# Kernel tuning notes

Measured on AMD Instinct MI355X. Metric: run time of the kernel, lower is better.

## Reference

```python
import jax, jax.numpy as jnp
import numpy as np

B, S, H = 32, 1024, 1024
W, K = 128, 6
NUM_HEADS = 16


def setup_inputs() -> dict:
    key = jax.random.key(0)
    k1, k2 = jax.random.split(key, 2)
    token_embeddings = jax.random.normal(k1, (B, S, H), dtype=jnp.float32)
    # nn.MultiheadAttention packed in_proj (q,k,v). v / out_proj never affect the
    # module output (attn_output is discarded), but we keep full-size params.
    in_proj_weight = jax.random.normal(k2, (3 * H, H), dtype=jnp.float32) * (1.0 / np.sqrt(H))
    in_proj_bias = jnp.zeros((3 * H,), dtype=jnp.float32)
    # Build ragged word->subtoken map as padded [B, W, K] indices + validity mask.
    # Words occupy disjoint contiguous slots (stride S//W = 8 >= K), matching the
    # disjointness the tokenizer guarantees in get_subtok_map.
    rng = np.random.default_rng(0)
    lengths = rng.integers(2, K + 1, size=(B, W))  # each kept word has >=2 subtokens
    stride = S // W
    base = (np.arange(W) * stride)[None, :, None] + np.arange(K)[None, None, :]
    base = np.broadcast_to(base, (B, W, K))
    mask = np.arange(K)[None, None, :] < lengths[:, :, None]
    idx = np.where(mask, base, 0)
    return {
        "token_embeddings": token_embeddings,
        "in_proj_weight": in_proj_weight,
        "in_proj_bias": in_proj_bias,
        "subtok_idx": jnp.asarray(idx, dtype=jnp.int32),
        "subtok_mask": jnp.asarray(mask),
        "num_heads": NUM_HEADS,
    }


def _merge(token_embeddings, in_proj_weight, in_proj_bias, subtok_idx, subtok_mask, num_heads):
    Bv, Sv, Hv = token_embeddings.shape
    Wv, Kv = subtok_idx.shape[1], subtok_idx.shape[2]
    hd = Hv // num_heads
    dtype = token_embeddings.dtype
    maskf = subtok_mask.astype(dtype)
    b_idx = jnp.arange(Bv)[:, None, None]
    sub = token_embeddings[b_idx, subtok_idx]                      # [B,W,K,H] gather
    x = (sub * maskf[..., None]).reshape(Bv * Wv, Kv, Hv)          # zero-padded groups
    # q,k projections (v / out_proj do not influence returned embeddings)
    qk = x @ in_proj_weight[: 2 * Hv].T + in_proj_bias[: 2 * Hv]
    q, k = qk[..., :Hv], qk[..., Hv:]
    q = q.reshape(-1, Kv, num_heads, hd).transpose(0, 2, 1, 3)     # [L,nh,K,hd]
    k = k.reshape(-1, Kv, num_heads, hd).transpose(0, 2, 1, 3)
    scores = jnp.einsum('lnqd,lnkd->lnqk', q, k) / jnp.asarray(np.sqrt(hd), dtype)
    m = maskf.reshape(-1, Kv)
    pair = m[:, :, None] * m[:, None, :]                           # [L,K,K] 0/1 float mask
    # torch adds float attn_mask to scores (it does NOT -inf mask here) -- faithful
    scores = scores + pair[:, None]
    attn = jax.nn.softmax(scores, axis=-1)
    w_mean = attn.mean(axis=1)                                     # avg over heads (need_weights)
    contrib = (pair * w_mean).sum(axis=1)                          # sum over query dim
    contrib = contrib / (contrib.sum(axis=-1, keepdims=True) + 1e-8)
    contrib = contrib.reshape(Bv, Wv, Kv)                          # zero at invalid k
    unified = jnp.einsum('bwkh,bwk->bwh', sub, contrib)
    # zero ALL subtoken positions of each word, then write merged vector at the
    # first subtoken index (equivalent to the torch in-place per-word loop since
    # word index sets are disjoint). Column Sv is a discard slot for padding.
    safe_idx = jnp.where(subtok_mask, subtok_idx, Sv)
    keep = jnp.ones((Bv, Sv + 1), dtype=dtype)
    keep = keep.at[b_idx, safe_idx].set(0.0)
    out = token_embeddings * keep[:, :Sv, None]
    out = jnp.concatenate([out, jnp.zeros((Bv, 1, Hv), dtype)], axis=1)
    first_idx = jnp.where(subtok_mask[:, :, 0], subtok_idx[:, :, 0], Sv)
    out = out.at[jnp.arange(Bv)[:, None], first_idx].set(unified)
    return out[:, :Sv]


def reference(token_embeddings, in_proj_weight, in_proj_bias, subtok_idx, subtok_mask, num_heads):
    return _merge(token_embeddings, in_proj_weight, in_proj_bias, subtok_idx, subtok_mask, num_heads)
```

## Files before the change

kernel.cpp:

```cpp
#include <hip/hip_runtime.h>
#include <hip/hip_bf16.h>
#include <stdint.h>
#include <stddef.h>

#define Bdim  32
#define Sdim  1024
#define Hdim  1024
#define Wdim  128
#define Ktok  6
#define NHEAD 16
#define HDdim 64
#define Lgrp  (Bdim*Wdim)
#define Mrows (Lgrp*Ktok)
#define Ncols (2*Hdim)
#define CVTROWS (Mrows + Ncols)

typedef __attribute__((ext_vector_type(8))) short short8;
typedef __attribute__((ext_vector_type(4))) short short4_t;
typedef __attribute__((ext_vector_type(4))) float floatx4;
typedef __hip_bfloat16 bf16_t;

typedef unsigned int u32_g __attribute__((address_space(1)));
typedef unsigned int u32_l __attribute__((address_space(3)));

__device__ __forceinline__ void gld_lds16(const void* g, void* l) {
    __builtin_amdgcn_global_load_lds((const u32_g*)g, (u32_l*)l, 16, 0, 0);
}

__device__ __forceinline__ float b2f(short s) {
    union { float f; unsigned u; } x; x.u = ((unsigned)(unsigned short)s) << 16; return x.f;
}

__device__ __forceinline__ short8 cvt8(const float4 lo, const float4 hi) {
    union { short8 s; bf16_t h[8]; } u;
    u.h[0] = __float2bfloat16(lo.x); u.h[1] = __float2bfloat16(lo.y);
    u.h[2] = __float2bfloat16(lo.z); u.h[3] = __float2bfloat16(lo.w);
    u.h[4] = __float2bfloat16(hi.x); u.h[5] = __float2bfloat16(hi.y);
    u.h[6] = __float2bfloat16(hi.z); u.h[7] = __float2bfloat16(hi.w);
    return u.s;
}

__global__ void gather_cvt(const float* __restrict__ TE, const float* __restrict__ Wt,
                           const int* __restrict__ sidx,
                           bf16_t* __restrict__ Xa, bf16_t* __restrict__ Wb)
{
    const int r = blockIdx.x;
    const int t = threadIdx.x;
    const float* src;
    bf16_t* dst;
    if (r < Mrows) {
        src = TE + ((size_t)(r/768)*Sdim + sidx[r])*Hdim;
        dst = Xa + (size_t)r*Hdim;
    } else {
        src = Wt + (size_t)(r - Mrows)*Hdim;
        dst = Wb + (size_t)(r - Mrows)*Hdim;
    }
    const float4 v = *(const float4*)(src + t*4);
    union { short4_t s; bf16_t h[4]; } u;
    u.h[0] = __float2bfloat16(v.x); u.h[1] = __float2bfloat16(v.y);
    u.h[2] = __float2bfloat16(v.z); u.h[3] = __float2bfloat16(v.w);
    *(short4_t*)(dst + t*4) = u.s;
}

__global__ __launch_bounds__(256, 2) void gemm_bf16(
    const bf16_t* __restrict__ Xa, const bf16_t* __restrict__ Wb,
    const float* __restrict__ bias, bf16_t* __restrict__ Cq)
{
    __shared__ __align__(16) bf16_t As[128*32];
    __shared__ __align__(16) bf16_t Bs[128*32];
    const int tid  = threadIdx.x;
    const int wv   = tid >> 6;
    const int lane = tid & 63;
    const int tileM = blockIdx.x * 128;
    const int tileN = blockIdx.y * 128;

    const int r0 = wv*32 + (lane>>2);
    const int r1 = r0 + 16;
    const int c8 = (lane&3)*8;

    const bf16_t* pA0 = Xa + (size_t)(tileM + r0)*Hdim + c8;
    const bf16_t* pA1 = Xa + (size_t)(tileM + r1)*Hdim + c8;
    const bf16_t* pB0 = Wb + (size_t)(tileN + r0)*Hdim + c8;
    const bf16_t* pB1 = Wb + (size_t)(tileN + r1)*Hdim + c8;
    bf16_t* lA0 = &As[r0*32 + c8];
    bf16_t* lA1 = &As[r1*32 + c8];
    bf16_t* lB0 = &Bs[r0*32 + c8];
    bf16_t* lB1 = &Bs[r1*32 + c8];

    const int wm = (wv & 1)*64;
    const int wn = (wv >> 1)*64;
    const int fr = lane & 15;
    const int fq = lane >> 4;

    floatx4 acc[4][4] = {};

    for (int k0 = 0; k0 < Hdim; k0 += 32) {
        gld_lds16(pA0 + k0, lA0);
        gld_lds16(pA1 + k0, lA1);
        gld_lds16(pB0 + k0, lB0);
        gld_lds16(pB1 + k0, lB1);
        __syncthreads();
        short8 a[4], b[4];
        #pragma unroll
        for (int mi = 0; mi < 4; mi++)
            a[mi] = *(const short8*)(const void*)&As[(wm + mi*16 + fr)*32 + fq*8];
        #pragma unroll
        for (int ni = 0; ni < 4; ni++)
            b[ni] = *(const short8*)(const void*)&Bs[(wn + ni*16 + fr)*32 + fq*8];
        #pragma unroll
        for (int mi = 0; mi < 4; mi++)
            #pragma unroll
            for (int ni = 0; ni < 4; ni++)
                acc[mi][ni] = __builtin_amdgcn_mfma_f32_16x16x32_bf16(
                    a[mi], b[ni], acc[mi][ni], 0, 0, 0);
        __syncthreads();
    }

    #pragma unroll
    for (int ni = 0; ni < 4; ni++) {
        const int col = tileN + wn + ni*16 + fr;
        const float bv = bias[col];
        #pragma unroll
        for (int mi = 0; mi < 4; mi++) {
            #pragma unroll
            for (int r = 0; r < 4; r++) {
                const int row = tileM + wm + mi*16 + fq*4 + r;
                Cq[(size_t)row * Ncols + col] = __float2bfloat16(acc[mi][ni][r] + bv);
            }
        }
    }
}

__global__ __launch_bounds__(256, 2) void gemm_qk(
    const float* __restrict__ TE, const float* __restrict__ Wt,
    const float* __restrict__ bias, const int* __restrict__ sidx,
    bf16_t* __restrict__ Cq)
{
    __shared__ __align__(16) bf16_t As[128*32];
    __shared__ __align__(16) bf16_t Bs[128*32];
    const int tid  = threadIdx.x;
    const int wv   = tid >> 6;
    const int lane = tid & 63;
    const int tileM = blockIdx.x * 128;
    const int tileN = blockIdx.y * 128;

    const int r0 = wv*32 + (lane>>2);
    const int r1 = r0 + 16;
    const int c8 = (lane&3)*8;

    const int m0 = tileM + r0;
    const int m1 = tileM + r1;
    const float* pA0 = TE + ((size_t)(m0/768)*Sdim + sidx[m0])*Hdim + c8;
    const float* pA1 = TE + ((size_t)(m1/768)*Sdim + sidx[m1])*Hdim + c8;
    const float* pB0 = Wt + (size_t)(tileN + r0)*Hdim + c8;
    const float* pB1 = Wt + (size_t)(tileN + r1)*Hdim + c8;
    bf16_t* lA0 = &As[r0*32 + c8];
    bf16_t* lA1 = &As[r1*32 + c8];
    bf16_t* lB0 = &Bs[r0*32 + c8];
    bf16_t* lB1 = &Bs[r1*32 + c8];

    const int wm = (wv & 1)*64;
    const int wn = (wv >> 1)*64;
    const int fr = lane & 15;
    const int fq = lane >> 4;

    floatx4 acc[4][4] = {};

    for (int k0 = 0; k0 < Hdim; k0 += 32) {
        const float4 a0l = *(const float4*)(pA0 + k0);
        const float4 a0h = *(const float4*)(pA0 + k0 + 4);
        const float4 a1l = *(const float4*)(pA1 + k0);
        const float4 a1h = *(const float4*)(pA1 + k0 + 4);
        const float4 b0l = *(const float4*)(pB0 + k0);
        const float4 b0h = *(const float4*)(pB0 + k0 + 4);
        const float4 b1l = *(const float4*)(pB1 + k0);
        const float4 b1h = *(const float4*)(pB1 + k0 + 4);
        *(short8*)(void*)lA0 = cvt8(a0l, a0h);
        *(short8*)(void*)lA1 = cvt8(a1l, a1h);
        *(short8*)(void*)lB0 = cvt8(b0l, b0h);
        *(short8*)(void*)lB1 = cvt8(b1l, b1h);
        __syncthreads();
        short8 a[4], b[4];
        #pragma unroll
        for (int mi = 0; mi < 4; mi++)
            a[mi] = *(const short8*)(const void*)&As[(wm + mi*16 + fr)*32 + fq*8];
        #pragma unroll
        for (int ni = 0; ni < 4; ni++)
            b[ni] = *(const short8*)(const void*)&Bs[(wn + ni*16 + fr)*32 + fq*8];
        #pragma unroll
        for (int mi = 0; mi < 4; mi++)
            #pragma unroll
            for (int ni = 0; ni < 4; ni++)
                acc[mi][ni] = __builtin_amdgcn_mfma_f32_16x16x32_bf16(
                    a[mi], b[ni], acc[mi][ni], 0, 0, 0);
        __syncthreads();
    }

    #pragma unroll
    for (int ni = 0; ni < 4; ni++) {
        const int col = tileN + wn + ni*16 + fr;
        const float bv = bias[col];
        #pragma unroll
        for (int mi = 0; mi < 4; mi++) {
            #pragma unroll
            for (int r = 0; r < 4; r++) {
                const int row = tileM + wm + mi*16 + fq*4 + r;
                Cq[(size_t)row * Ncols + col] = __float2bfloat16(acc[mi][ni][r] + bv);
            }
        }
    }
}

__global__ void copy_te(const uint4* __restrict__ src, uint4* __restrict__ dst, int n)
{
    int i = blockIdx.x * blockDim.x + threadIdx.x;
    const int stride = gridDim.x * blockDim.x;
    for (; i < n; i += stride) dst[i] = src[i];
}

__global__ __launch_bounds__(256) void attn_merge(
    const float* __restrict__ TE, const bf16_t* __restrict__ Cq,
    const float* __restrict__ bias, const int* __restrict__ sidx,
    float* __restrict__ out)
{
    __shared__ __align__(16) bf16_t qk[Ktok][Ncols];
    __shared__ float sc[NHEAD][Ktok][Ktok];
    __shared__ float cN[Ktok];
    __shared__ int   validS[Ktok];

    const int g   = blockIdx.x;
    const int b   = g >> 7;
    const int w   = g & (Wdim - 1);
    const int tid = threadIdx.x;

    if (tid < Ktok) {
        const int id = sidx[g*Ktok + tid];
        validS[tid] = (id != 0) || (w == 0 && tid == 0);
    }
    __syncthreads();

    int valid[Ktok], idxv[Ktok];
    #pragma unroll
    for (int kk = 0; kk < Ktok; kk++) { valid[kk] = validS[kk]; idxv[kk] = sidx[g*Ktok + kk]; }

    #pragma unroll
    for (int it = 0; it < Ktok; it++) {
        if (valid[it]) {
            *(short8*)(void*)&qk[it][tid*8] =
                *(const short8*)(const void*)&Cq[(size_t)(g*Ktok + it)*Ncols + tid*8];
        } else {
            const float4 lo = *(const float4*)(bias + tid*8);
            const float4 hi = *(const float4*)(bias + tid*8 + 4);
            *(short8*)(void*)&qk[it][tid*8] = cvt8(lo, hi);
        }
    }
    __syncthreads();

    for (int t = tid; t < NHEAD*Ktok*Ktok; t += 256) {
        const int n = t / (Ktok*Ktok);
        const int pr = t % (Ktok*Ktok);
        const int i = pr / Ktok, j = pr % Ktok;
        const bf16_t* qp = &qk[i][n*HDdim];
        const bf16_t* kp = &qk[j][Hdim + n*HDdim];
        float dot = 0.f;
        #pragma unroll
        for (int c = 0; c < 8; c++) {
            const short8 q8 = *(const short8*)(const void*)(qp + c*8);
            const short8 k8 = *(const short8*)(const void*)(kp + c*8);
            #pragma unroll
            for (int e = 0; e < 8; e++) dot += b2f(q8[e]) * b2f(k8[e]);
        }
        sc[n][i][j] = dot * 0.125f + ((valid[i] && valid[j]) ? 1.0f : 0.0f);
    }
    __syncthreads();

    if (tid < NHEAD*Ktok) {
        const int n = tid / Ktok, i = tid % Ktok;
        float mx = -1e30f;
        #pragma unroll
        for (int j = 0; j < Ktok; j++) mx = fmaxf(mx, sc[n][i][j]);
        float e[Ktok], sum = 0.f;
        #pragma unroll
        for (int j = 0; j < Ktok; j++) { e[j] = __expf(sc[n][i][j] - mx); sum += e[j]; }
        const float inv = 1.0f / sum;
        #pragma unroll
        for (int j = 0; j < Ktok; j++) sc[n][i][j] = e[j] * inv;
    }
    __syncthreads();

    if (tid == 0) {
        float cb[Ktok], tot = 0.f;
        #pragma unroll
        for (int j = 0; j < Ktok; j++) cb[j] = 0.f;
        #pragma unroll
        for (int i = 0; i < Ktok; i++) {
            if (!valid[i]) continue;
            #pragma unroll
            for (int j = 0; j < Ktok; j++) {
                if (!valid[j]) continue;
                float s = 0.f;
                #pragma unroll
                for (int n = 0; n < NHEAD; n++) s += sc[n][i][j];
                cb[j] += s * (1.0f/NHEAD);
            }
        }
        #pragma unroll
        for (int j = 0; j < Ktok; j++) tot += cb[j];
        const float inv = 1.0f / (tot + 1e-8f);
        #pragma unroll
        for (int j = 0; j < Ktok; j++) cN[j] = cb[j] * inv;
    }
    __syncthreads();

    float cw[Ktok];
    #pragma unroll
    for (int kk = 0; kk < Ktok; kk++) cw[kk] = cN[kk];

    const int c4 = tid * 4;
    const size_t rowOut = ((size_t)b*Sdim + idxv[0]) * Hdim;
    float4 u = {0.f, 0.f, 0.f, 0.f};
    #pragma unroll
    for (int kk = 0; kk < Ktok; kk++) {
        const float4 v = *(const float4*)(TE + ((size_t)b*Sdim + idxv[kk])*Hdim + c4);
        u.x += cw[kk]*v.x; u.y += cw[kk]*v.y; u.z += cw[kk]*v.z; u.w += cw[kk]*v.w;
    }
    *(float4*)(out + rowOut + c4) = u;

    const float4 z = {0.f, 0.f, 0.f, 0.f};
    #pragma unroll
    for (int kk = 1; kk < Ktok; kk++) {
        if (valid[kk]) {
            *(float4*)(out + ((size_t)b*Sdim + idxv[kk])*Hdim + c4) = z;
        }
    }
}

extern "C" void kernel_launch(void* const* d_in, const int* in_sizes, int n_in,
                              void* d_out, int out_size, void* d_ws, size_t ws_size,
                              hipStream_t stream)
{
    (void)in_sizes; (void)n_in; (void)out_size;
    const float* TE   = (const float*)d_in[0];
    const float* Wt   = (const float*)d_in[1];
    const float* bias = (const float*)d_in[2];
    const int*   sidx = (const int*)d_in[3];
    float*  out  = (float*)d_out;

    const size_t CQ_BYTES = (size_t)Mrows * Ncols * 2;
    const size_t XA_BYTES = (size_t)Mrows * Hdim * 2;
    const size_t WB_BYTES = (size_t)Ncols * Hdim * 2;
    bf16_t* Cq = (bf16_t*)d_ws;
    bf16_t* Xa = (bf16_t*)((char*)d_ws + CQ_BYTES);
    bf16_t* Wb = (bf16_t*)((char*)d_ws + CQ_BYTES + XA_BYTES);

    dim3 gg(Mrows/128, Ncols/128);
    if (ws_size >= CQ_BYTES + XA_BYTES + WB_BYTES) {
        gather_cvt<<<CVTROWS, 256, 0, stream>>>(TE, Wt, sidx, Xa, Wb);
        gemm_bf16<<<gg, dim3(256), 0, stream>>>(Xa, Wb, bias, Cq);
    } else {
        gemm_qk<<<gg, dim3(256), 0, stream>>>(TE, Wt, bias, sidx, Cq);
    }
    copy_te<<<4096, 256, 0, stream>>>((const uint4*)TE, (uint4*)d_out,
                                      (Bdim*Sdim*Hdim)/4);
    attn_merge<<<Lgrp, 256, 0, stream>>>(TE, Cq, bias, sidx, out);
}
```

Before: 469.6 us.

## Replace bf16 GEMM with 256x256 double-buffered 8-phase pipelined kernel

Replaces the 128x128, BK=32 single-buffered GEMM with a 512-thread, 256x256x64 tile kernel. It double-buffers LDS, splits each K step into four quadrant phases that interleave async global->LDS staging with MFMA work, and swizzles LDS addresses to avoid bank conflicts. It also remaps block indices for L2 locality and raises MFMA issue priority. The goal is to hide global load latency and cut per-iteration barrier stalls in the QK projection GEMM, at the cost of far more LDS per block (128 KB) and more register pressure, which may lower occupancy.

Measured after the change: 418.6 us. -10.9%, faster.

```diff
diff --git a/kernel.cpp b/kernel.cpp
--- a/kernel.cpp
+++ b/kernel.cpp
@@ -15,6 +15,11 @@
 #define Ncols (2*Hdim)
 #define CVTROWS (Mrows + Ncols)
 
+#define BMg 256
+#define BNg 256
+#define BKg 64
+#define NKT (Hdim/BKg)
+
 typedef __attribute__((ext_vector_type(8))) short short8;
 typedef __attribute__((ext_vector_type(4))) short short4_t;
 typedef __attribute__((ext_vector_type(4))) float floatx4;
@@ -38,6 +43,19 @@
     u.h[4] = __float2bfloat16(hi.x); u.h[5] = __float2bfloat16(hi.y);
     u.h[6] = __float2bfloat16(hi.z); u.h[7] = __float2bfloat16(hi.w);
     return u.s;
+}
+
+__device__ __forceinline__ int lds_ro(int row, int col) {
+    const int sub = ((row >> 4) << 1) | (col >> 5);
+    const int c   = (col & 31) ^ (((row >> 3) & 1) << 4);
+    return (sub << 10) | ((row & 15) << 6) | (c << 1);
+}
+__device__ __forceinline__ void stg_map(int p, int& row, int& col) {
+    const int r16 = (p >> 6) & 15;
+    int c = (p >> 1) & 31;
+    c ^= ((r16 >> 3) & 1) << 4;
+    row = ((p >> 11) << 4) | r16;
+    col = (((p >> 10) & 1) << 5) | c;
 }
 
 __global__ void gather_cvt(const float* __restrict__ TE, const float* __restrict__ Wt,
@@ -62,73 +80,150 @@
     *(short4_t*)(dst + t*4) = u.s;
 }
 
-__global__ __launch_bounds__(256, 2) void gemm_bf16(
+__global__ __launch_bounds__(512, 2) void gemm_8ph(
     const bf16_t* __restrict__ Xa, const bf16_t* __restrict__ Wb,
     const float* __restrict__ bias, bf16_t* __restrict__ Cq)
 {
-    __shared__ __align__(16) bf16_t As[128*32];
-    __shared__ __align__(16) bf16_t Bs[128*32];
+    __shared__ __align__(16) char lds[2][2][2][16384];
     const int tid  = threadIdx.x;
+    const int lane = tid & 63;
     const int wv   = tid >> 6;
-    const int lane = tid & 63;
-    const int tileM = blockIdx.x * 128;
-    const int tileN = blockIdx.y * 128;
-
-    const int r0 = wv*32 + (lane>>2);
-    const int r1 = r0 + 16;
-    const int c8 = (lane&3)*8;
-
-    const bf16_t* pA0 = Xa + (size_t)(tileM + r0)*Hdim + c8;
-    const bf16_t* pA1 = Xa + (size_t)(tileM + r1)*Hdim + c8;
-    const bf16_t* pB0 = Wb + (size_t)(tileN + r0)*Hdim + c8;
-    const bf16_t* pB1 = Wb + (size_t)(tileN + r1)*Hdim + c8;
-    bf16_t* lA0 = &As[r0*32 + c8];
-    bf16_t* lA1 = &As[r1*32 + c8];
-    bf16_t* lB0 = &Bs[r0*32 + c8];
-    bf16_t* lB1 = &Bs[r1*32 + c8];
-
-    const int wm = (wv & 1)*64;
-    const int wn = (wv >> 1)*64;
-    const int fr = lane & 15;
-    const int fq = lane >> 4;
-
-    floatx4 acc[4][4] = {};
-
-    for (int k0 = 0; k0 < Hdim; k0 += 32) {
-        gld_lds16(pA0 + k0, lA0);
-        gld_lds16(pA1 + k0, lA1);
-        gld_lds16(pB0 + k0, lB0);
-        gld_lds16(pB1 + k0, lB1);
-        __syncthreads();
-        short8 a[4], b[4];
-        #pragma unroll
-        for (int mi = 0; mi < 4; mi++)
-            a[mi] = *(const short8*)(const void*)&As[(wm + mi*16 + fr)*32 + fq*8];
-        #pragma unroll
-        for (int ni = 0; ni < 4; ni++)
-            b[ni] = *(const short8*)(const void*)&Bs[(wn + ni*16 + fr)*32 + fq*8];
-        #pragma unroll
-        for (int mi = 0; mi < 4; mi++)
+    const int wr   = wv >> 2;
+    const int wc   = wv & 3;
+    const int fr   = lane & 15;
+    const int fq   = lane >> 4;
+
+    const int cpx  = gridDim.x >> 3;
+    const int orig = blockIdx.x;
+    const int swz  = (orig & 7) * cpx + (orig >> 3);
+    const int tileM = (swz >> 3) * BMg;
+    const int tileN = (swz & 7) * BNg;
+
+    int r0, c0, r1, c1;
+    stg_map(tid * 16, r0, c0);
+    stg_map(8192 + tid * 16, r1, c1);
+
+    const bf16_t* srcA = Xa + (size_t)tileM * Hdim;
+    const bf16_t* srcB = Wb + (size_t)tileN * Hdim;
+
+    int aoff[4][2], boff[2][2];
+    #pragma unroll
+    for (int mi = 0; mi < 4; mi++)
+        #pragma unroll
+        for (int ks = 0; ks < 2; ks++)
+            aoff[mi][ks] = lds_ro(wr*64 + mi*16 + fr, ks*32 + fq*8);
+    #pragma unroll
+    for (int ni = 0; ni < 2; ni++)
+        #pragma unroll
+        for (int ks = 0; ks < 2; ks++)
+            boff[ni][ks] = lds_ro(wc*32 + ni*16 + fr, ks*32 + fq*8);
+
+    short8 a[4][2], b[2][2];
+    floatx4 acc[2][2][4][2] = {};
+
+#define STAGE(bufi, isB, half, kt) do { \
+        const bf16_t* _s = (isB) ? srcB : srcA; \
+        char* _d = &lds[(bufi)][(isB)][(half)][0]; \
+        const int _kb = (kt) * BKg; \
+        gld_lds16(_s + (size_t)((half)*128 + r0) * Hdim + _kb + c0, _d + tid*16); \
+        gld_lds16(_s + (size_t)((half)*128 + r1) * Hdim + _kb + c1, _d + 8192 + tid*16); \
+    } while (0)
+
+#define LDAf(bufi, qr) do { \
+        const char* _sA = &lds[(bufi)][0][(qr)][0]; \
+        _Pragma("unroll") \
+        for (int mi = 0; mi < 4; mi++) { \
+            a[mi][0] = *(const short8*)(const void*)(_sA + aoff[mi][0]); \
+            a[mi][1] = *(const short8*)(const void*)(_sA + aoff[mi][1]); \
+        } \
+    } while (0)
+
+#define LDBf(bufi, qc) do { \
+        const char* _sB = &lds[(bufi)][1][(qc)][0]; \
+        _Pragma("unroll") \
+        for (int ni = 0; ni < 2; ni++) { \
+            b[ni][0] = *(const short8*)(const void*)(_sB + boff[ni][0]); \
+            b[ni][1] = *(const short8*)(const void*)(_sB + boff[ni][1]); \
+        } \
+    } while (0)
+
+#define MMA(qr, qc) do { \
+        __builtin_amdgcn_s_setprio(1); \
+        _Pragma("unroll") \
+        for (int mi = 0; mi < 4; mi++) \
+            _Pragma("unroll") \
+            for (int ni = 0; ni < 2; ni++) { \
+                acc[qr][qc][mi][ni] = __builtin_amdgcn_mfma_f32_16x16x32_bf16( \
+                    a[mi][0], b[ni][0], acc[qr][qc][mi][ni], 0, 0, 0); \
+                acc[qr][qc][mi][ni] = __builtin_amdgcn_mfma_f32_16x16x32_bf16( \
+                    a[mi][1], b[ni][1], acc[qr][qc][mi][ni], 0, 0, 0); \
+            } \
+        __builtin_amdgcn_s_setprio(0); \
+    } while (0)
+
+#define WAIT_LGKM() asm volatile("s_waitcnt lgkmcnt(0)" ::: "memory")
+
+    STAGE(0, 0, 0, 0);
+    STAGE(0, 1, 1, 0);
+    STAGE(0, 0, 1, 0);
+    STAGE(0, 1, 0, 0);
+    STAGE(1, 0, 0, 1);
+    STAGE(1, 1, 1, 1);
+    asm volatile("s_waitcnt vmcnt(4)" ::: "memory");
+    __builtin_amdgcn_s_barrier();
+
+    for (int u = 0; u < NKT; ++u) {
+        const int bf = u & 1;
+        const int nb = bf ^ 1;
+        LDAf(bf, 0); LDBf(bf, 0);
+        if (u + 1 < NKT) STAGE(nb, 0, 1, u + 1);
+        __builtin_amdgcn_s_barrier();
+        WAIT_LGKM();
+        MMA(0, 0);
+        __builtin_amdgcn_s_barrier();
+        LDBf(bf, 1);
+        if (u + 1 < NKT) STAGE(nb, 1, 0, u + 1);
+        __builtin_amdgcn_s_barrier();
+        WAIT_LGKM();
+        MMA(0, 1);
+        __builtin_amdgcn_s_barrier();
+        LDAf(bf, 1);
+        if (u + 2 < NKT) STAGE(bf, 0, 0, u + 2);
+        __builtin_amdgcn_s_barrier();
+        WAIT_LGKM();
+        MMA(1, 1);
+        __builtin_amdgcn_s_barrier();
+        LDBf(bf, 0);
+        if (u + 2 < NKT) STAGE(bf, 1, 1, u + 2);
+        __builtin_amdgcn_s_barrier();
+        WAIT_LGKM();
+        MMA(1, 0);
+        if (u + 2 < NKT)      asm volatile("s_waitcnt vmcnt(4)" ::: "memory");
+        else if (u + 1 < NKT) asm volatile("s_waitcnt vmcnt(0)" ::: "memory");
+        __builtin_amdgcn_s_barrier();
+    }
+
+    #pragma unroll
+    for (int qr = 0; qr < 2; qr++)
+      #pragma unroll
+      for (int qc = 0; qc < 2; qc++)
+        #pragma unroll
+        for (int ni = 0; ni < 2; ni++) {
+            const int col = tileN + qc*128 + wc*32 + ni*16 + fr;
+            const float bv = bias[col];
             #pragma unroll
-            for (int ni = 0; ni < 4; ni++)
-                acc[mi][ni] = __builtin_amdgcn_mfma_f32_16x16x32_bf16(
-                    a[mi], b[ni], acc[mi][ni], 0, 0, 0);
-        __syncthreads();
-    }
-
-    #pragma unroll
-    for (int ni = 0; ni < 4; ni++) {
-        const int col = tileN + wn + ni*16 + fr;
-        const float bv = bias[col];
-        #pragma unroll
-        for (int mi = 0; mi < 4; mi++) {
-            #pragma unroll
-            for (int r = 0; r < 4; r++) {
-                const int row = tileM + wm + mi*16 + fq*4 + r;
-                Cq[(size_t)row * Ncols + col] = __float2bfloat16(acc[mi][ni][r] + bv);
-            }
-        }
-    }
+            for (int mi = 0; mi < 4; mi++)
+              #pragma unroll
+              for (int j = 0; j < 4; j++) {
+                const int row = tileM + qr*128 + wr*64 + mi*16 + fq*4 + j;
+                Cq[(size_t)row * Ncols + col] = __float2bfloat16(acc[qr][qc][mi][ni][j] + bv);
+              }
+        }
+#undef STAGE
+#undef LDAf
+#undef LDBf
+#undef MMA
+#undef WAIT_LGKM
 }
 
 __global__ __launch_bounds__(256, 2) void gemm_qk(
@@ -353,11 +448,11 @@
     bf16_t* Xa = (bf16_t*)((char*)d_ws + CQ_BYTES);
     bf16_t* Wb = (bf16_t*)((char*)d_ws + CQ_BYTES + XA_BYTES);
 
-    dim3 gg(Mrows/128, Ncols/128);
     if (ws_size >= CQ_BYTES + XA_BYTES + WB_BYTES) {
         gather_cvt<<<CVTROWS, 256, 0, stream>>>(TE, Wt, sidx, Xa, Wb);
-        gemm_bf16<<<gg, dim3(256), 0, stream>>>(Xa, Wb, bias, Cq);
+        gemm_8ph<<<dim3((Mrows/BMg)*(Ncols/BNg)), dim3(512), 0, stream>>>(Xa, Wb, bias, Cq);
     } else {
+        dim3 gg(Mrows/128, Ncols/128);
         gemm_qk<<<gg, dim3(256), 0, stream>>>(TE, Wt, bias, sidx, Cq);
     }
     copy_te<<<4096, 256, 0, stream>>>((const uint4*)TE, (uint4*)d_out,
```
